# Kernel optimization log

Measured on AMD Instinct MI355X. Metric: run time of the kernel, lower is better.

Reference implementation:

```python
import jax, jax.numpy as jnp
import numpy as np

NU, NI, E = 50000, 20000, 400000
IN, HID, OUT = 128, 256, 128
NEG_SLOPE_ATTN = 0.2   # DGL GATConv default
NEG_SLOPE_ACT = 0.01   # F.leaky_relu default
BN_EPS = 1e-5


def setup_inputs() -> dict:
    key = jax.random.key(0)
    ks = jax.random.split(key, 32)
    d = {}
    d["x_user"] = jax.random.normal(ks[0], (NU, IN), jnp.float32)
    d["x_item"] = jax.random.normal(ks[1], (NI, IN), jnp.float32)
    d["eu"] = jax.random.randint(ks[2], (E,), 0, NU, jnp.int32)
    d["ei"] = jax.random.randint(ks[3], (E,), 0, NI, jnp.int32)
    i = 4
    dims = [(IN, 4, 64), (HID, 4, 64), (HID, 4, 64), (HID, 4, 32)]
    for L, (fin, H, dh) in enumerate(dims):
        for rel in ("ui", "iu"):
            d[f"W{L}_{rel}"] = jax.random.normal(ks[i], (fin, H * dh), jnp.float32) * 0.1; i += 1
            d[f"A{L}_{rel}"] = jax.random.normal(ks[i], (2, H, dh), jnp.float32) * 0.1; i += 1
    # BN params: [layer, (gamma,beta), HID]; gamma near 1, beta near 0
    gu = 1.0 + 0.05 * jax.random.normal(ks[i], (3, 1, HID), jnp.float32); i += 1
    bu = 0.05 * jax.random.normal(ks[i], (3, 1, HID), jnp.float32); i += 1
    gi = 1.0 + 0.05 * jax.random.normal(ks[i], (3, 1, HID), jnp.float32); i += 1
    bi = 0.05 * jax.random.normal(ks[i], (3, 1, HID), jnp.float32); i += 1
    d["bn_u"] = jnp.concatenate([gu, bu], axis=1)
    d["bn_i"] = jnp.concatenate([gi, bi], axis=1)
    return d


def _gat(x_src, x_dst, W, A, src, dst, n_dst):
    # Single-relation bipartite GATConv (DGL semantics).
    H, dh = A.shape[1], A.shape[2]
    hs = (x_src @ W).reshape(-1, H, dh)           # [Ns,H,dh]
    hd = (x_dst @ W).reshape(-1, H, dh)           # [Nd,H,dh]
    el = jnp.einsum('nhd,hd->nh', hs, A[0])
    er = jnp.einsum('nhd,hd->nh', hd, A[1])
    e = jax.nn.leaky_relu(el[src] + er[dst], NEG_SLOPE_ATTN)   # [E,H]
    emax = jax.ops.segment_max(e, dst, num_segments=n_dst)
    ee = jnp.exp(e - emax[dst])
    denom = jax.ops.segment_sum(ee, dst, num_segments=n_dst)
    alpha = ee / denom[dst]                       # segment softmax over in-edges
    out = jax.ops.segment_sum(hs[src] * alpha[..., None], dst, num_segments=n_dst)
    return out.reshape(n_dst, H * dh)


def _bn(x, gamma, beta):
    mu = x.mean(axis=0)
    var = x.var(axis=0)   # biased, matches torch BN normalization
    return gamma * (x - mu) * jax.lax.rsqrt(var + BN_EPS) + beta


def reference(x_user, x_item, eu, ei, W0_ui, W0_iu, A0_ui, A0_iu,
              W1_ui, W1_iu, A1_ui, A1_iu, W2_ui, W2_iu, A2_ui, A2_iu,
              W3_ui, W3_iu, A3_ui, A3_iu, bn_u, bn_i):
    Wui = [W0_ui, W1_ui, W2_ui]; Aui = [A0_ui, A1_ui, A2_ui]
    Wiu = [W0_iu, W1_iu, W2_iu]; Aiu = [A0_iu, A1_iu, A2_iu]
    hu, hi = x_user, x_item
    for L in range(3):
        ni = _gat(hu, hi, Wui[L], Aui[L], eu, ei, NI)   # user -> item
        nu = _gat(hi, hu, Wiu[L], Aiu[L], ei, eu, NU)   # item -> user
        nu = _bn(nu, bn_u[L, 0], bn_u[L, 1])
        ni = _bn(ni, bn_i[L, 0], bn_i[L, 1])
        if L == 2:   # last hidden layer uses tanh in non-residual path
            hu, hi = jnp.tanh(nu), jnp.tanh(ni)
        else:
            hu = jax.nn.leaky_relu(nu, NEG_SLOPE_ACT)
            hi = jax.nn.leaky_relu(ni, NEG_SLOPE_ACT)
    out_i = _gat(hu, hi, W3_ui, A3_ui, eu, ei, NI)
    out_u = _gat(hi, hu, W3_iu, A3_iu, ei, eu, NU)
    return jnp.concatenate([out_u, out_i], axis=0)   # [NU+NI, OUT]
```

## Files before the change

### kernel.cpp

```cpp
#include <hip/hip_runtime.h>

#define NUSERS 50000
#define NITEMS 20000
#define NEDGES 400000

typedef _Float16 f16;
typedef __attribute__((ext_vector_type(8))) _Float16 f16x8;
typedef __attribute__((ext_vector_type(4))) _Float16 f16x4;
typedef __attribute__((ext_vector_type(2))) _Float16 f16x2;
typedef __attribute__((ext_vector_type(4))) float f32x4;

__global__ void prep_k(const float* __restrict__ Wa, const float* __restrict__ Aa,
                       f16* __restrict__ Bta, float* __restrict__ efa,
                       const float* __restrict__ Wb, const float* __restrict__ Ab,
                       f16* __restrict__ Btb, float* __restrict__ efb,
                       int K, int Nw, int dh) {
  int t = blockIdx.x * blockDim.x + threadIdx.x;
  int half = K * Nw;
  if (t >= 2 * half) return;
  const float* W = (t < half) ? Wa : Wb;
  const float* A = (t < half) ? Aa : Ab;
  f16* Bt = (t < half) ? Bta : Btb;
  float* ef = (t < half) ? efa : efb;
  int t2 = (t < half) ? t : t - half;
  int n = t2 / K, k = t2 - n * K;
  Bt[t2] = (f16)W[(long)k * Nw + n];
  if (t2 < K * 8) {
    int j = t2 / (K * 4);
    int r = t2 - j * K * 4;
    int h = r / K, f = r - h * K;
    const float* Aj = A + j * Nw;
    float s = 0.f;
    for (int d = 0; d < dh; ++d) s += W[f * Nw + h * dh + d] * Aj[h * dh + d];
    ef[j * 4 * K + h * K + f] = s;
  }
}

__global__ void xcvt_k(const float* __restrict__ xu, f16* __restrict__ yu, long nu,
                       const float* __restrict__ xi, f16* __restrict__ yi, long ni) {
  long i = (long)blockIdx.x * blockDim.x + threadIdx.x;
  if (i < nu) yu[i] = (f16)xu[i];
  else if (i < nu + ni) yi[i - nu] = (f16)xi[i - nu];
}

__global__ __launch_bounds__(256) void hgemm2_k(const f16* __restrict__ Aa, const f16* __restrict__ Bta,
                                                f16* __restrict__ Ca, int Ma, int gya,
                                                const f16* __restrict__ Ab, const f16* __restrict__ Btb,
                                                f16* __restrict__ Cb, int Mb,
                                                int N, int K) {
  __shared__ f16 As[128 * 32];
  __shared__ f16 Bs[128 * 32];
  int by = blockIdx.y;
  const f16* A; const f16* Bt; f16* C; int M; int row0;
  if (by < gya) { A = Aa; Bt = Bta; C = Ca; M = Ma; row0 = by * 128; }
  else          { A = Ab; Bt = Btb; C = Cb; M = Mb; row0 = (by - gya) * 128; }
  int tid = threadIdx.x;
  int col0 = blockIdx.x * 128;
  int lane = tid & 63, wv = tid >> 6;
  int wr = (wv & 1) * 64, wc = (wv >> 1) * 64;
  int l16 = lane & 15, q = lane >> 4;
  f32x4 acc[4][4] = {};
  int r = tid >> 2, c8 = (tid & 3) * 8;
  for (int k0 = 0; k0 < K; k0 += 32) {
    int ra = min(row0 + r, M - 1);
    uint4 va = *(const uint4*)&A[(long)ra * K + k0 + c8];
    int ra2 = min(row0 + r + 64, M - 1);
    uint4 va2 = *(const uint4*)&A[(long)ra2 * K + k0 + c8];
    uint4 vb = *(const uint4*)&Bt[(long)(col0 + r) * K + k0 + c8];
    uint4 vb2 = *(const uint4*)&Bt[(long)(col0 + r + 64) * K + k0 + c8];
    *(uint4*)&As[r * 32 + c8] = va;
    *(uint4*)&As[(r + 64) * 32 + c8] = va2;
    *(uint4*)&Bs[r * 32 + c8] = vb;
    *(uint4*)&Bs[(r + 64) * 32 + c8] = vb2;
    __syncthreads();
    f16x8 af[4], bfr[4];
#pragma unroll
    for (int i = 0; i < 4; ++i) {
      af[i] = *(const f16x8*)&As[(wr + i * 16 + l16) * 32 + q * 8];
      bfr[i] = *(const f16x8*)&Bs[(wc + i * 16 + l16) * 32 + q * 8];
    }
#pragma unroll
    for (int i = 0; i < 4; ++i)
#pragma unroll
      for (int j = 0; j < 4; ++j)
        acc[i][j] = __builtin_amdgcn_mfma_f32_16x16x32_f16(af[i], bfr[j], acc[i][j], 0, 0, 0);
    __syncthreads();
  }
#pragma unroll
  for (int i = 0; i < 4; ++i) {
#pragma unroll
    for (int reg = 0; reg < 4; ++reg) {
      int rr = row0 + wr + i * 16 + q * 4 + reg;
      if (rr < M) {
#pragma unroll
        for (int j = 0; j < 4; ++j)
          C[(long)rr * N + col0 + wc + j * 16 + l16] = (f16)acc[i][j][reg];
      }
    }
  }
}

__global__ __launch_bounds__(256) void eler_k(
    const f16* __restrict__ hbu, const float* __restrict__ ef_ui, const float* __restrict__ ef_iu,
    float* __restrict__ el_u, float* __restrict__ er_u,
    const f16* __restrict__ hbi, float* __restrict__ el_i, float* __restrict__ er_i, int K) {
  __shared__ float xs[256];
  int b = blockIdx.x, t = threadIdx.x;
  const f16* hb; const float* elf; const float* erf; float* el; float* er; int n;
  if (b < NUSERS) { hb = hbu; elf = ef_ui; erf = ef_iu + 4 * K; el = el_u; er = er_u; n = b; }
  else            { hb = hbi; elf = ef_iu; erf = ef_ui + 4 * K; el = el_i; er = er_i; n = b - NUSERS; }
  if (t < K) xs[t] = (float)hb[(long)n * K + t];
  __syncthreads();
  int j = t >> 5, l = t & 31;
  const float* fr = (j < 4) ? (elf + j * K) : (erf + (j - 4) * K);
  float p = 0.f;
  for (int f = l; f < K; f += 32) p += xs[f] * fr[f];
#pragma unroll
  for (int off = 16; off; off >>= 1) p += __shfl_down(p, off, 32);
  if (l == 0) { if (j < 4) el[n * 4 + j] = p; else er[n * 4 + (j - 4)] = p; }
}

__global__ void hist_k(const int* __restrict__ ei, int* __restrict__ degi,
                       const int* __restrict__ eu, int* __restrict__ degu) {
  int e = blockIdx.x * blockDim.x + threadIdx.x;
  if (e < NEDGES) atomicAdd(&degi[ei[e]], 1);
  else if (e < 2 * NEDGES) atomicAdd(&degu[eu[e - NEDGES]], 1);
}

__global__ __launch_bounds__(256) void scan1_k(const int* __restrict__ deg,
                                               int* __restrict__ bsum, int N) {
  __shared__ int red[256];
  int base = blockIdx.x * 1024, t = threadIdx.x;
  int s = 0;
#pragma unroll
  for (int j = 0; j < 4; ++j) { int i = base + t * 4 + j; s += (i < N) ? deg[i] : 0; }
  red[t] = s; __syncthreads();
  for (int off = 128; off; off >>= 1) { if (t < off) red[t] += red[t + off]; __syncthreads(); }
  if (t == 0) bsum[blockIdx.x] = red[0];
}

__global__ void scan2_k(int* __restrict__ bsum, int nb) {
  if (threadIdx.x == 0) {
    int run = 0;
    for (int i = 0; i < nb; ++i) { int v = bsum[i]; bsum[i] = run; run += v; }
  }
}

__global__ __launch_bounds__(256) void scan3_k(const int* __restrict__ deg,
                                               const int* __restrict__ bsum,
                                               int* __restrict__ rowptr, int N) {
  __shared__ int tsum[256];
  int base = blockIdx.x * 1024, t = threadIdx.x;
  int v[4]; int s = 0;
#pragma unroll
  for (int j = 0; j < 4; ++j) { int i = base + t * 4 + j; v[j] = (i < N) ? deg[i] : 0; s += v[j]; }
  tsum[t] = s; __syncthreads();
  for (int off = 1; off < 256; off <<= 1) {
    int x = (t >= off) ? tsum[t - off] : 0;
    __syncthreads();
    tsum[t] += x;
    __syncthreads();
  }
  int run = bsum[blockIdx.x] + ((t > 0) ? tsum[t - 1] : 0);
#pragma unroll
  for (int j = 0; j < 4; ++j) {
    int i = base + t * 4 + j;
    if (i < N) rowptr[i] = run;
    run += v[j];
  }
}

__global__ void setval_k(int* __restrict__ p, int v) { *p = v; }

__global__ void copy2_k(const int* __restrict__ a, int* __restrict__ b, int Na,
                        const int* __restrict__ c, int* __restrict__ d, int Nc) {
  int i = blockIdx.x * blockDim.x + threadIdx.x;
  if (i < Na) b[i] = a[i];
  else if (i < Na + Nc) d[i - Na] = c[i - Na];
}

__global__ void scat_k(const int* __restrict__ ei, const int* __restrict__ eu,
                       int* __restrict__ curi, int* __restrict__ srci,
                       int* __restrict__ curu, int* __restrict__ srcu) {
  int e = blockIdx.x * blockDim.x + threadIdx.x;
  if (e < NEDGES) {
    int p = atomicAdd(&curi[ei[e]], 1);
    srci[p] = eu[e];
  } else if (e < 2 * NEDGES) {
    int e2 = e - NEDGES;
    int p = atomicAdd(&curu[eu[e2]], 1);
    srcu[p] = ei[e2];
  }
}

template <int W, int DH, typename OUT>
__global__ __launch_bounds__(256) void agg_k(
    const float* __restrict__ elA, const float* __restrict__ erA,
    const int* __restrict__ rpA, const int* __restrict__ srcA,
    const f16* __restrict__ hsA, OUT* __restrict__ outA, int nA,
    const float* __restrict__ elB, const float* __restrict__ erB,
    const int* __restrict__ rpB, const int* __restrict__ srcB,
    const f16* __restrict__ hsB, OUT* __restrict__ outB, int nB) {
  constexpr int CPL = W >> 6;
  constexpr int SHIFT = (W == 256) ? 9 : 8;
  constexpr bool OF16 = (sizeof(OUT) == 2);
  __shared__ float alds[4][256];
  __shared__ int soff[4][64];
  int wv = threadIdx.x >> 6;
  int g = blockIdx.x * 4 + wv;
  int lane = threadIdx.x & 63;
  const float* el; const float* er; const int* rp; const int* srcv;
  const f16* hs; OUT* outp; int d;
  if (g < nA)           { el = elA; er = erA; rp = rpA; srcv = srcA; hs = hsA; outp = outA; d = g; }
  else if (g < nA + nB) { el = elB; er = erB; rp = rpB; srcv = srcB; hs = hsB; outp = outB; d = g - nA; }
  else return;
  int s0 = rp[d], s1 = rp[d + 1];
  int deg = s1 - s0;
  int c0 = lane * CPL;
  int h = c0 / DH;
  long obase = (long)d * W + c0;
  if (deg == 0) {
#pragma unroll
    for (int q = 0; q < CPL; ++q) outp[obase + q] = (OUT)0.f;
    return;
  }
  const float NEG = -3.0e38f;
  float acc[CPL];
#pragma unroll
  for (int q = 0; q < CPL; ++q) acc[q] = 0.f;
  float inv;

  if (deg <= 64) {
    int hh = lane & 3, p = lane >> 2;
    float er_h = er[d * 4 + hh];
    float vv[4];
    float vmax = NEG;
#pragma unroll
    for (int j = 0; j < 4; ++j) {
      int slot = j * 16 + p;
      vv[j] = NEG;
      if (slot < deg) {
        int sj = srcv[s0 + slot];
        if (hh == 0) soff[wv][slot] = sj << SHIFT;
        float v = el[sj * 4 + hh] + er_h;
        v = v > 0.f ? v : 0.2f * v;
        vv[j] = v;
        vmax = fmaxf(vmax, v);
      }
    }
#pragma unroll
    for (int off = 4; off < 64; off <<= 1) vmax = fmaxf(vmax, __shfl_xor(vmax, off, 64));
    float ssum = 0.f;
#pragma unroll
    for (int j = 0; j < 4; ++j) {
      int slot = j * 16 + p;
      if (slot < deg) {
        float e = expf(vv[j] - vmax);
        alds[wv][slot * 4 + hh] = e;
        ssum += e;
      }
    }
#pragma unroll
    for (int off = 4; off < 64; off <<= 1) ssum += __shfl_xor(ssum, off, 64);
    float Sh = __shfl(ssum, (lane & ~3) | h, 64);
    inv = 1.0f / Sh;
    const char* hbase = (const char*)hs + (size_t)c0 * sizeof(f16);
    for (int j = 0; j < deg; ++j) {
      float aj = alds[wv][j * 4 + h];
      int off = soff[wv][j];
      const f16* row = (const f16*)(hbase + (size_t)(unsigned)off);
      if constexpr (CPL == 4) {
        f16x4 hv = *(const f16x4*)row;
        acc[0] += aj * (float)hv[0]; acc[1] += aj * (float)hv[1];
        acc[2] += aj * (float)hv[2]; acc[3] += aj * (float)hv[3];
      } else {
        f16x2 hv = *(const f16x2*)row;
        acc[0] += aj * (float)hv[0]; acc[1] += aj * (float)hv[1];
      }
    }
  } else {
    float4 er4 = *(const float4*)&er[d * 4];
    float m0 = NEG, m1 = NEG, m2 = NEG, m3 = NEG;
    for (int k = s0 + lane; k < s1; k += 64) {
      int s = srcv[k];
      float4 e4 = *(const float4*)&el[s * 4];
      float v;
      v = e4.x + er4.x; v = v > 0.f ? v : 0.2f * v; m0 = fmaxf(m0, v);
      v = e4.y + er4.y; v = v > 0.f ? v : 0.2f * v; m1 = fmaxf(m1, v);
      v = e4.z + er4.z; v = v > 0.f ? v : 0.2f * v; m2 = fmaxf(m2, v);
      v = e4.w + er4.w; v = v > 0.f ? v : 0.2f * v; m3 = fmaxf(m3, v);
    }
#pragma unroll
    for (int off = 32; off; off >>= 1) {
      m0 = fmaxf(m0, __shfl_xor(m0, off, 64));
      m1 = fmaxf(m1, __shfl_xor(m1, off, 64));
      m2 = fmaxf(m2, __shfl_xor(m2, off, 64));
      m3 = fmaxf(m3, __shfl_xor(m3, off, 64));
    }
    float S0 = 0.f, S1 = 0.f, S2 = 0.f, S3 = 0.f;
    for (int k = s0 + lane; k < s1; k += 64) {
      int s = srcv[k];
      float4 e4 = *(const float4*)&el[s * 4];
      float v;
      v = e4.x + er4.x; v = v > 0.f ? v : 0.2f * v; S0 += expf(v - m0);
      v = e4.y + er4.y; v = v > 0.f ? v : 0.2f * v; S1 += expf(v - m1);
      v = e4.z + er4.z; v = v > 0.f ? v : 0.2f * v; S2 += expf(v - m2);
      v = e4.w + er4.w; v = v > 0.f ? v : 0.2f * v; S3 += expf(v - m3);
    }
#pragma unroll
    for (int off = 32; off; off >>= 1) {
      S0 += __shfl_xor(S0, off, 64);
      S1 += __shfl_xor(S1, off, 64);
      S2 += __shfl_xor(S2, off, 64);
      S3 += __shfl_xor(S3, off, 64);
    }
    float mh = h == 0 ? m0 : h == 1 ? m1 : h == 2 ? m2 : m3;
    float Sh = h == 0 ? S0 : h == 1 ? S1 : h == 2 ? S2 : S3;
    float erh = h == 0 ? er4.x : h == 1 ? er4.y : h == 2 ? er4.z : er4.w;
    inv = 1.0f / Sh;
    for (int k = s0; k < s1; ++k) {
      int s = srcv[k];
      float v = el[s * 4 + h] + erh; v = v > 0.f ? v : 0.2f * v;
      float a = expf(v - mh);
      const f16* row = &hs[(long)s * W + c0];
      if constexpr (CPL == 4) {
        f16x4 hv = *(const f16x4*)row;
        acc[0] += a * (float)hv[0]; acc[1] += a * (float)hv[1];
        acc[2] += a * (float)hv[2]; acc[3] += a * (float)hv[3];
      } else {
        f16x2 hv = *(const f16x2*)row;
        acc[0] += a * (float)hv[0]; acc[1] += a * (float)hv[1];
      }
    }
  }
  if constexpr (OF16) {
    if constexpr (CPL == 4) {
      f16x4 o = { (f16)(acc[0] * inv), (f16)(acc[1] * inv), (f16)(acc[2] * inv), (f16)(acc[3] * inv) };
      *(f16x4*)&outp[obase] = o;
    } else {
      f16x2 o = { (f16)(acc[0] * inv), (f16)(acc[1] * inv) };
      *(f16x2*)&outp[obase] = o;
    }
  } else {
    if constexpr (CPL == 4) {
      *(float4*)&outp[obase] = make_float4(acc[0] * inv, acc[1] * inv, acc[2] * inv, acc[3] * inv);
    } else {
      *(float2*)&outp[obase] = make_float2(acc[0] * inv, acc[1] * inv);
    }
  }
}

__global__ void zero2_k(float* __restrict__ a, float* __restrict__ b) {
  int t = threadIdx.x;
  a[t] = 0.f; b[t] = 0.f;
}

__global__ __launch_bounds__(256) void bn_stats2_k(const f16* __restrict__ xu, float* __restrict__ su, int Nu, int gU,
                                                   const f16* __restrict__ xi, float* __restrict__ si, int Ni) {
  const int C = 256;
  int b = blockIdx.x;
  const f16* x; float* sums; int N; int r0;
  if (b < gU) { x = xu; sums = su; N = Nu; r0 = b * 64; }
  else        { x = xi; sums = si; N = Ni; r0 = (b - gU) * 64; }
  int c = threadIdx.x;
  int r1 = min(r0 + 64, N);
  float s = 0.f, s2 = 0.f;
  for (int r = r0; r < r1; ++r) {
    float v = (float)x[(long)r * C + c];
    s += v; s2 += v * v;
  }
  atomicAdd(&sums[c], s);
  atomicAdd(&sums[C + c], s2);
}

__global__ __launch_bounds__(256) void bn_fused_k(
    const f16* __restrict__ xu, const float* __restrict__ su, const float* __restrict__ gbu,
    f16* __restrict__ yu, int Nu,
    const f16* __restrict__ xi, const float* __restrict__ si, const float* __restrict__ gbi,
    f16* __restrict__ yi, int Ni,
    const float* __restrict__ efu, const float* __restrict__ efiu,
    float* __restrict__ el_u, float* __restrict__ er_u,
    float* __restrict__ el_i, float* __restrict__ er_i, int act) {
  const int Kn = 256;
  __shared__ float xs[256];
  int b = blockIdx.x, t = threadIdx.x;
  const f16* x; const float* sums; const float* gb; f16* y; int n; int N;
  const float* elf; const float* erf; float* el; float* er;
  if (b < Nu) { x = xu; sums = su; gb = gbu; y = yu; n = b; N = Nu; elf = efu;  erf = efiu + 4 * Kn; el = el_u; er = er_u; }
  else        { x = xi; sums = si; gb = gbi; y = yi; n = b - Nu; N = Ni; elf = efiu; erf = efu + 4 * Kn;  el = el_i; er = er_i; }
  long base = (long)n * 256;
  float val = (float)x[base + t];
  float inv_n = 1.0f / (float)N;
  float mean = sums[t] * inv_n;
  float var = sums[256 + t] * inv_n - mean * mean;
  float v = gb[t] * (val - mean) * rsqrtf(var + 1e-5f) + gb[256 + t];
  v = act ? tanhf(v) : (v > 0.f ? v : 0.01f * v);
  y[base + t] = (f16)v;
  xs[t] = v;
  __syncthreads();
  int j = t >> 5, l = t & 31;
  const float* fr = (j < 4) ? (elf + j * Kn) : (erf + (j - 4) * Kn);
  float p = 0.f;
  for (int f = l; f < Kn; f += 32) p += xs[f] * fr[f];
#pragma unroll
  for (int off = 16; off; off >>= 1) p += __shfl_down(p, off, 32);
  if (l == 0) { if (j < 4) el[n * 4 + j] = p; else er[n * 4 + (j - 4)] = p; }
}

extern "C" void kernel_launch(void* const* d_in, const int* in_sizes, int n_in,
                              void* d_out, int out_size, void* d_ws, size_t ws_size,
                              hipStream_t stream) {
  const float* x_user = (const float*)d_in[0];
  const float* x_item = (const float*)d_in[1];
  const int* eu = (const int*)d_in[2];
  const int* ei = (const int*)d_in[3];
  const float *Wm[4][2], *Am[4][2];
  for (int L = 0; L < 4; ++L) {
    Wm[L][0] = (const float*)d_in[4 + L * 4 + 0];
    Am[L][0] = (const float*)d_in[4 + L * 4 + 1];
    Wm[L][1] = (const float*)d_in[4 + L * 4 + 2];
    Am[L][1] = (const float*)d_in[4 + L * 4 + 3];
  }
  const float* bnu = (const float*)d_in[20];
  const float* bni = (const float*)d_in[21];
  float* out = (float*)d_out;

  float* ws = (float*)d_ws;
  size_t o = 0;
  float* el_u = ws + o; o += (size_t)NUSERS * 4;
  float* er_u = ws + o; o += (size_t)NUSERS * 4;
  float* el_i = ws + o; o += (size_t)NITEMS * 4;
  float* er_i = ws + o; o += (size_t)NITEMS * 4;
  float* ef_all[4][2];
  for (int L = 0; L < 4; ++L)
    for (int rl = 0; rl < 2; ++rl) { ef_all[L][rl] = ws + o; o += 2048; }
  float* bns_u = ws + o; o += 512;
  float* bns_i = ws + o; o += 512;
  f16* hb_u   = (f16*)(ws + o); o += (size_t)NUSERS * 128;
  f16* hb_i   = (f16*)(ws + o); o += (size_t)NITEMS * 128;
  f16* hsb_u  = (f16*)(ws + o); o += (size_t)NUSERS * 128;
  f16* hsb_i  = (f16*)(ws + o); o += (size_t)NITEMS * 128;
  f16* aggh_u = (f16*)(ws + o); o += (size_t)NUSERS * 128;
  f16* aggh_i = (f16*)(ws + o); o += (size_t)NITEMS * 128;
  f16* Bt_all[4][2];
  for (int L = 0; L < 4; ++L) {
    int K = (L == 0) ? 128 : 256;
    int W = (L == 3) ? 128 : 256;
    for (int rl = 0; rl < 2; ++rl) { Bt_all[L][rl] = (f16*)(ws + o); o += (size_t)K * W / 2; }
  }
  int* deg_i    = (int*)(ws + o); o += NITEMS;
  int* deg_u    = (int*)(ws + o); o += NUSERS;
  int* rowptr_i = (int*)(ws + o); o += NITEMS + 1;
  int* rowptr_u = (int*)(ws + o); o += NUSERS + 1;
  int* cur_i    = (int*)(ws + o); o += NITEMS;
  int* cur_u    = (int*)(ws + o); o += NUSERS;
  int* bsum     = (int*)(ws + o); o += 256;
  int* csrsrc_i = (int*)(ws + o); o += NEDGES;
  int* csrsrc_u = (int*)(ws + o); o += NEDGES;

  const int gE2 = (2 * NEDGES + 255) / 256;
  const int nb_i = (NITEMS + 1023) / 1024;
  const int nb_u = (NUSERS + 1023) / 1024;
  const int gU = (NUSERS + 63) / 64;
  const int gI = (NITEMS + 63) / 64;

  hipMemsetAsync(deg_i, 0, (NITEMS + NUSERS) * sizeof(int), stream);
  hist_k<<<dim3(gE2), dim3(256), 0, stream>>>(ei, deg_i, eu, deg_u);
  scan1_k<<<dim3(nb_i), dim3(256), 0, stream>>>(deg_i, bsum, NITEMS);
  scan2_k<<<dim3(1), dim3(64), 0, stream>>>(bsum, nb_i);
  scan3_k<<<dim3(nb_i), dim3(256), 0, stream>>>(deg_i, bsum, rowptr_i, NITEMS);
  setval_k<<<dim3(1), dim3(1), 0, stream>>>(rowptr_i + NITEMS, NEDGES);
  scan1_k<<<dim3(nb_u), dim3(256), 0, stream>>>(deg_u, bsum, NUSERS);
  scan2_k<<<dim3(1), dim3(64), 0, stream>>>(bsum, nb_u);
  scan3_k<<<dim3(nb_u), dim3(256), 0, stream>>>(deg_u, bsum, rowptr_u, NUSERS);
  setval_k<<<dim3(1), dim3(1), 0, stream>>>(rowptr_u + NUSERS, NEDGES);
  copy2_k<<<dim3((NITEMS + NUSERS + 255) / 256), dim3(256), 0, stream>>>(rowptr_i, cur_i, NITEMS, rowptr_u, cur_u, NUSERS);
  scat_k<<<dim3(gE2), dim3(256), 0, stream>>>(ei, eu, cur_i, csrsrc_i, cur_u, csrsrc_u);

  for (int L = 0; L < 4; ++L) {
    int K = (L == 0) ? 128 : 256;
    int dh = (L == 3) ? 32 : 64;
    int W = 4 * dh;
    prep_k<<<dim3((2 * K * W + 255) / 256), dim3(256), 0, stream>>>(
        Wm[L][0], Am[L][0], Bt_all[L][0], ef_all[L][0],
        Wm[L][1], Am[L][1], Bt_all[L][1], ef_all[L][1], K, W, dh);
  }

  xcvt_k<<<dim3(((NUSERS + NITEMS) * 128 + 255) / 256), dim3(256), 0, stream>>>(
      x_user, hb_u, (long)NUSERS * 128, x_item, hb_i, (long)NITEMS * 128);
  eler_k<<<dim3(NUSERS + NITEMS), dim3(256), 0, stream>>>(
      hb_u, ef_all[0][0], ef_all[0][1], el_u, er_u, hb_i, el_i, er_i, 128);

  int K = 128;
  for (int L = 0; L < 4; ++L) {
    const int dh = (L == 3) ? 32 : 64;
    const int W = 4 * dh;

    const int gya = (NUSERS + 127) / 128, gyb = (NITEMS + 127) / 128;
    hgemm2_k<<<dim3(W / 128, gya + gyb), dim3(256), 0, stream>>>(
        hb_u, Bt_all[L][0], hsb_u, NUSERS, gya, hb_i, Bt_all[L][1], hsb_i, NITEMS, W, K);

    const int gAgg = (NITEMS + NUSERS + 3) / 4;
    if (L < 3) {
      agg_k<256, 64, f16><<<dim3(gAgg), dim3(256), 0, stream>>>(
          el_u, er_i, rowptr_i, csrsrc_i, hsb_u, aggh_i, NITEMS,
          el_i, er_u, rowptr_u, csrsrc_u, hsb_i, aggh_u, NUSERS);
      zero2_k<<<dim3(1), dim3(512), 0, stream>>>(bns_u, bns_i);
      bn_stats2_k<<<dim3(gU + gI), dim3(256), 0, stream>>>(aggh_u, bns_u, NUSERS, gU, aggh_i, bns_i, NITEMS);
      bn_fused_k<<<dim3(NUSERS + NITEMS), dim3(256), 0, stream>>>(
          aggh_u, bns_u, bnu + L * 512, hb_u, NUSERS,
          aggh_i, bns_i, bni + L * 512, hb_i, NITEMS,
          ef_all[L + 1][0], ef_all[L + 1][1],
          el_u, er_u, el_i, er_i, L == 2);
      K = 256;
    } else {
      agg_k<128, 32, float><<<dim3(gAgg), dim3(256), 0, stream>>>(
          el_u, er_i, rowptr_i, csrsrc_i, hsb_u, out + (size_t)NUSERS * 128, NITEMS,
          el_i, er_u, rowptr_u, csrsrc_u, hsb_i, out, NUSERS);
    }
  }
}
```

Before: 917.6 us.

## Fuse BN statistics into aggregation and merge small setup kernels

Batch-norm sum and sum-of-squares are now accumulated inside the aggregation kernel, first in shared memory and then with atomics spread over four partial buffers, so the separate stats pass that re-read the aggregated features is gone. The input fp16 conversion is folded into the layer-0 attention-logit kernel, and the rowptr end write and cursor copy are folded into the scan kernels. This removes several launches and one full read of the activations per layer, at the cost of shared-memory atomics and an extra barrier in the aggregation kernel.

```diff
diff --git a/kernel.cpp b/kernel.cpp
--- a/kernel.cpp
+++ b/kernel.cpp
@@ -34,13 +34,6 @@
     for (int d = 0; d < dh; ++d) s += W[f * Nw + h * dh + d] * Aj[h * dh + d];
     ef[j * 4 * K + h * K + f] = s;
   }
-}
-
-__global__ void xcvt_k(const float* __restrict__ xu, f16* __restrict__ yu, long nu,
-                       const float* __restrict__ xi, f16* __restrict__ yi, long ni) {
-  long i = (long)blockIdx.x * blockDim.x + threadIdx.x;
-  if (i < nu) yu[i] = (f16)xu[i];
-  else if (i < nu + ni) yi[i - nu] = (f16)xi[i - nu];
 }
 
 __global__ __launch_bounds__(256) void hgemm2_k(const f16* __restrict__ Aa, const f16* __restrict__ Bta,
@@ -100,16 +93,23 @@
   }
 }
 
-__global__ __launch_bounds__(256) void eler_k(
-    const f16* __restrict__ hbu, const float* __restrict__ ef_ui, const float* __restrict__ ef_iu,
+__global__ __launch_bounds__(256) void eler0_k(
+    const float* __restrict__ xu, f16* __restrict__ hbu,
+    const float* __restrict__ ef_ui, const float* __restrict__ ef_iu,
     float* __restrict__ el_u, float* __restrict__ er_u,
-    const f16* __restrict__ hbi, float* __restrict__ el_i, float* __restrict__ er_i, int K) {
-  __shared__ float xs[256];
+    const float* __restrict__ xi, f16* __restrict__ hbi,
+    float* __restrict__ el_i, float* __restrict__ er_i) {
+  const int K = 128;
+  __shared__ float xs[128];
   int b = blockIdx.x, t = threadIdx.x;
-  const f16* hb; const float* elf; const float* erf; float* el; float* er; int n;
-  if (b < NUSERS) { hb = hbu; elf = ef_ui; erf = ef_iu + 4 * K; el = el_u; er = er_u; n = b; }
-  else            { hb = hbi; elf = ef_iu; erf = ef_ui + 4 * K; el = el_i; er = er_i; n = b - NUSERS; }
-  if (t < K) xs[t] = (float)hb[(long)n * K + t];
+  const float* x; f16* hb; const float* elf; const float* erf; float* el; float* er; int n;
+  if (b < NUSERS) { x = xu; hb = hbu; elf = ef_ui; erf = ef_iu + 4 * K; el = el_u; er = er_u; n = b; }
+  else            { x = xi; hb = hbi; elf = ef_iu; erf = ef_ui + 4 * K; el = el_i; er = er_i; n = b - NUSERS; }
+  if (t < K) {
+    f16 xv = (f16)x[(long)n * K + t];
+    hb[(long)n * K + t] = xv;
+    xs[t] = (float)xv;
+  }
   __syncthreads();
   int j = t >> 5, l = t & 31;
   const float* fr = (j < 4) ? (elf + j * K) : (erf + (j - 4) * K);
@@ -139,16 +139,18 @@
   if (t == 0) bsum[blockIdx.x] = red[0];
 }
 
-__global__ void scan2_k(int* __restrict__ bsum, int nb) {
+__global__ void scan2_k(int* __restrict__ bsum, int nb, int* __restrict__ endp, int endv) {
   if (threadIdx.x == 0) {
     int run = 0;
     for (int i = 0; i < nb; ++i) { int v = bsum[i]; bsum[i] = run; run += v; }
+    *endp = endv;
   }
 }
 
 __global__ __launch_bounds__(256) void scan3_k(const int* __restrict__ deg,
                                                const int* __restrict__ bsum,
-                                               int* __restrict__ rowptr, int N) {
+                                               int* __restrict__ rowptr,
+                                               int* __restrict__ cur, int N) {
   __shared__ int tsum[256];
   int base = blockIdx.x * 1024, t = threadIdx.x;
   int v[4]; int s = 0;
@@ -165,18 +167,9 @@
 #pragma unroll
   for (int j = 0; j < 4; ++j) {
     int i = base + t * 4 + j;
-    if (i < N) rowptr[i] = run;
+    if (i < N) { rowptr[i] = run; cur[i] = run; }
     run += v[j];
   }
-}
-
-__global__ void setval_k(int* __restrict__ p, int v) { *p = v; }
-
-__global__ void copy2_k(const int* __restrict__ a, int* __restrict__ b, int Na,
-                        const int* __restrict__ c, int* __restrict__ d, int Nc) {
-  int i = blockIdx.x * blockDim.x + threadIdx.x;
-  if (i < Na) b[i] = a[i];
-  else if (i < Na + Nc) d[i - Na] = c[i - Na];
 }
 
 __global__ void scat_k(const int* __restrict__ ei, const int* __restrict__ eu,
@@ -193,184 +186,194 @@
   }
 }
 
-template <int W, int DH, typename OUT>
+template <int W, int DH, typename OUT, bool STATS>
 __global__ __launch_bounds__(256) void agg_k(
     const float* __restrict__ elA, const float* __restrict__ erA,
     const int* __restrict__ rpA, const int* __restrict__ srcA,
-    const f16* __restrict__ hsA, OUT* __restrict__ outA, int nA,
+    const f16* __restrict__ hsA, OUT* __restrict__ outA, int nA, int gA,
+    float* __restrict__ bnsA,
     const float* __restrict__ elB, const float* __restrict__ erB,
     const int* __restrict__ rpB, const int* __restrict__ srcB,
-    const f16* __restrict__ hsB, OUT* __restrict__ outB, int nB) {
+    const f16* __restrict__ hsB, OUT* __restrict__ outB, int nB,
+    float* __restrict__ bnsB) {
   constexpr int CPL = W >> 6;
   constexpr int SHIFT = (W == 256) ? 9 : 8;
   constexpr bool OF16 = (sizeof(OUT) == 2);
   __shared__ float alds[4][256];
   __shared__ int soff[4][64];
-  int wv = threadIdx.x >> 6;
-  int g = blockIdx.x * 4 + wv;
-  int lane = threadIdx.x & 63;
-  const float* el; const float* er; const int* rp; const int* srcv;
-  const f16* hs; OUT* outp; int d;
-  if (g < nA)           { el = elA; er = erA; rp = rpA; srcv = srcA; hs = hsA; outp = outA; d = g; }
-  else if (g < nA + nB) { el = elB; er = erB; rp = rpB; srcv = srcB; hs = hsB; outp = outB; d = g - nA; }
-  else return;
-  int s0 = rp[d], s1 = rp[d + 1];
-  int deg = s1 - s0;
+  __shared__ float sst[2][256];
+  int tid = threadIdx.x;
+  int wv = tid >> 6;
+  int lane = tid & 63;
+  bool sideA = (blockIdx.x < gA);
+  const float* el = sideA ? elA : elB;
+  const float* er = sideA ? erA : erB;
+  const int* rp   = sideA ? rpA : rpB;
+  const int* srcv = sideA ? srcA : srcB;
+  const f16* hs   = sideA ? hsA : hsB;
+  OUT* outp       = sideA ? outA : outB;
+  float* bns      = sideA ? bnsA : bnsB;
+  int n           = sideA ? nA : nB;
+  int d = (sideA ? blockIdx.x : blockIdx.x - gA) * 4 + wv;
+  bool active = (d < n);
+
+  if constexpr (STATS) {
+    sst[0][tid] = 0.f; sst[1][tid] = 0.f;
+    __syncthreads();
+  }
+
+  const float NEG = -3.0e38f;
+  float acc[CPL];
+#pragma unroll
+  for (int q = 0; q < CPL; ++q) acc[q] = 0.f;
+  float inv = 0.f;
   int c0 = lane * CPL;
   int h = c0 / DH;
+  int s0 = 0, deg = 0;
+  if (active) { s0 = rp[d]; deg = rp[d + 1] - s0; }
+
+  if (active && deg > 0) {
+    if (deg <= 64) {
+      int hh = lane & 3, p = lane >> 2;
+      float er_h = er[d * 4 + hh];
+      float vv[4];
+      float vmax = NEG;
+#pragma unroll
+      for (int j = 0; j < 4; ++j) {
+        int slot = j * 16 + p;
+        vv[j] = NEG;
+        if (slot < deg) {
+          int sj = srcv[s0 + slot];
+          if (hh == 0) soff[wv][slot] = sj << SHIFT;
+          float v = el[sj * 4 + hh] + er_h;
+          v = v > 0.f ? v : 0.2f * v;
+          vv[j] = v;
+          vmax = fmaxf(vmax, v);
+        }
+      }
+#pragma unroll
+      for (int off = 4; off < 64; off <<= 1) vmax = fmaxf(vmax, __shfl_xor(vmax, off, 64));
+      float ssum = 0.f;
+#pragma unroll
+      for (int j = 0; j < 4; ++j) {
+        int slot = j * 16 + p;
+        if (slot < deg) {
+          float e = expf(vv[j] - vmax);
+          alds[wv][slot * 4 + hh] = e;
+          ssum += e;
+        }
+      }
+#pragma unroll
+      for (int off = 4; off < 64; off <<= 1) ssum += __shfl_xor(ssum, off, 64);
+      float Sh = __shfl(ssum, (lane & ~3) | h, 64);
+      inv = 1.0f / Sh;
+      const char* hbase = (const char*)hs + (size_t)c0 * sizeof(f16);
+      for (int j = 0; j < deg; ++j) {
+        float aj = alds[wv][j * 4 + h];
+        int off = soff[wv][j];
+        const f16* row = (const f16*)(hbase + (size_t)(unsigned)off);
+        if constexpr (CPL == 4) {
+          f16x4 hv = *(const f16x4*)row;
+          acc[0] += aj * (float)hv[0]; acc[1] += aj * (float)hv[1];
+          acc[2] += aj * (float)hv[2]; acc[3] += aj * (float)hv[3];
+        } else {
+          f16x2 hv = *(const f16x2*)row;
+          acc[0] += aj * (float)hv[0]; acc[1] += aj * (float)hv[1];
+        }
+      }
+    } else {
+      float4 er4 = *(const float4*)&er[d * 4];
+      float m0 = NEG, m1 = NEG, m2 = NEG, m3 = NEG;
+      for (int k = s0 + lane; k < s0 + deg; k += 64) {
+        int s = srcv[k];
+        float4 e4 = *(const float4*)&el[s * 4];
+        float v;
+        v = e4.x + er4.x; v = v > 0.f ? v : 0.2f * v; m0 = fmaxf(m0, v);
+        v = e4.y + er4.y; v = v > 0.f ? v : 0.2f * v; m1 = fmaxf(m1, v);
+        v = e4.z + er4.z; v = v > 0.f ? v : 0.2f * v; m2 = fmaxf(m2, v);
+        v = e4.w + er4.w; v = v > 0.f ? v : 0.2f * v; m3 = fmaxf(m3, v);
+      }
+#pragma unroll
+      for (int off = 32; off; off >>= 1) {
+        m0 = fmaxf(m0, __shfl_xor(m0, off, 64));
+        m1 = fmaxf(m1, __shfl_xor(m1, off, 64));
+        m2 = fmaxf(m2, __shfl_xor(m2, off, 64));
+        m3 = fmaxf(m3, __shfl_xor(m3, off, 64));
+      }
+      float S0 = 0.f, S1 = 0.f, S2 = 0.f, S3 = 0.f;
+      for (int k = s0 + lane; k < s0 + deg; k += 64) {
+        int s = srcv[k];
+        float4 e4 = *(const float4*)&el[s * 4];
+        float v;
+        v = e4.x + er4.x; v = v > 0.f ? v : 0.2f * v; S0 += expf(v - m0);
+        v = e4.y + er4.y; v = v > 0.f ? v : 0.2f * v; S1 += expf(v - m1);
+        v = e4.z + er4.z; v = v > 0.f ? v : 0.2f * v; S2 += expf(v - m2);
+        v = e4.w + er4.w; v = v > 0.f ? v : 0.2f * v; S3 += expf(v - m3);
+      }
+#pragma unroll
+      for (int off = 32; off; off >>= 1) {
+        S0 += __shfl_xor(S0, off, 64);
+        S1 += __shfl_xor(S1, off, 64);
+        S2 += __shfl_xor(S2, off, 64);
+        S3 += __shfl_xor(S3, off, 64);
+      }
+      float mh = h == 0 ? m0 : h == 1 ? m1 : h == 2 ? m2 : m3;
+      float Sh = h == 0 ? S0 : h == 1 ? S1 : h == 2 ? S2 : S3;
+      float erh = h == 0 ? er4.x : h == 1 ? er4.y : h == 2 ? er4.z : er4.w;
+      inv = 1.0f / Sh;
+      for (int k = s0; k < s0 + deg; ++k) {
+        int s = srcv[k];
+        float v = el[s * 4 + h] + erh; v = v > 0.f ? v : 0.2f * v;
+        float a = expf(v - mh);
+        const f16* row = &hs[(long)s * W + c0];
+        if constexpr (CPL == 4) {
+          f16x4 hv = *(const f16x4*)row;
+          acc[0] += a * (float)hv[0]; acc[1] += a * (float)hv[1];
+          acc[2] += a * (float)hv[2]; acc[3] += a * (float)hv[3];
+        } else {
+          f16x2 hv = *(const f16x2*)row;
+          acc[0] += a * (float)hv[0]; acc[1] += a * (float)hv[1];
+        }
+      }
+    }
+  }
+
   long obase = (long)d * W + c0;
-  if (deg == 0) {
-#pragma unroll
-    for (int q = 0; q < CPL; ++q) outp[obase + q] = (OUT)0.f;
-    return;
-  }
-  const float NEG = -3.0e38f;
-  float acc[CPL];
-#pragma unroll
-  for (int q = 0; q < CPL; ++q) acc[q] = 0.f;
-  float inv;
-
-  if (deg <= 64) {
-    int hh = lane & 3, p = lane >> 2;
-    float er_h = er[d * 4 + hh];
-    float vv[4];
-    float vmax = NEG;
-#pragma unroll
-    for (int j = 0; j < 4; ++j) {
-      int slot = j * 16 + p;
-      vv[j] = NEG;
-      if (slot < deg) {
-        int sj = srcv[s0 + slot];
-        if (hh == 0) soff[wv][slot] = sj << SHIFT;
-        float v = el[sj * 4 + hh] + er_h;
-        v = v > 0.f ? v : 0.2f * v;
-        vv[j] = v;
-        vmax = fmaxf(vmax, v);
+  float vq[CPL];
+  if (active) {
+    if constexpr (OF16) {
+      if constexpr (CPL == 4) {
+        f16x4 o;
+#pragma unroll
+        for (int q = 0; q < 4; ++q) { o[q] = (f16)(acc[q] * inv); vq[q] = (float)o[q]; }
+        *(f16x4*)&outp[obase] = o;
+      } else {
+        f16x2 o;
+#pragma unroll
+        for (int q = 0; q < 2; ++q) { o[q] = (f16)(acc[q] * inv); vq[q] = (float)o[q]; }
+        *(f16x2*)&outp[obase] = o;
+      }
+    } else {
+      if constexpr (CPL == 4) {
+        *(float4*)&outp[obase] = make_float4(acc[0] * inv, acc[1] * inv, acc[2] * inv, acc[3] * inv);
+      } else {
+        *(float2*)&outp[obase] = make_float2(acc[0] * inv, acc[1] * inv);
       }
     }
-#pragma unroll
-    for (int off = 4; off < 64; off <<= 1) vmax = fmaxf(vmax, __shfl_xor(vmax, off, 64));
-    float ssum = 0.f;
-#pragma unroll
-    for (int j = 0; j < 4; ++j) {
-      int slot = j * 16 + p;
-      if (slot < deg) {
-        float e = expf(vv[j] - vmax);
-        alds[wv][slot * 4 + hh] = e;
-        ssum += e;
+  }
+  if constexpr (STATS) {
+    if (active) {
+#pragma unroll
+      for (int q = 0; q < CPL; ++q) {
+        atomicAdd(&sst[0][c0 + q], vq[q]);
+        atomicAdd(&sst[1][c0 + q], vq[q] * vq[q]);
       }
     }
-#pragma unroll
-    for (int off = 4; off < 64; off <<= 1) ssum += __shfl_xor(ssum, off, 64);
-    float Sh = __shfl(ssum, (lane & ~3) | h, 64);
-    inv = 1.0f / Sh;
-    const char* hbase = (const char*)hs + (size_t)c0 * sizeof(f16);
-    for (int j = 0; j < deg; ++j) {
-      float aj = alds[wv][j * 4 + h];
-      int off = soff[wv][j];
-      const f16* row = (const f16*)(hbase + (size_t)(unsigned)off);
-      if constexpr (CPL == 4) {
-        f16x4 hv = *(const f16x4*)row;
-        acc[0] += aj * (float)hv[0]; acc[1] += aj * (float)hv[1];
-        acc[2] += aj * (float)hv[2]; acc[3] += aj * (float)hv[3];
-      } else {
-        f16x2 hv = *(const f16x2*)row;
-        acc[0] += aj * (float)hv[0]; acc[1] += aj * (float)hv[1];
-      }
-    }
-  } else {
-    float4 er4 = *(const float4*)&er[d * 4];
-    float m0 = NEG, m1 = NEG, m2 = NEG, m3 = NEG;
-    for (int k = s0 + lane; k < s1; k += 64) {
-      int s = srcv[k];
-      float4 e4 = *(const float4*)&el[s * 4];
-      float v;
-      v = e4.x + er4.x; v = v > 0.f ? v : 0.2f * v; m0 = fmaxf(m0, v);
-      v = e4.y + er4.y; v = v > 0.f ? v : 0.2f * v; m1 = fmaxf(m1, v);
-      v = e4.z + er4.z; v = v > 0.f ? v : 0.2f * v; m2 = fmaxf(m2, v);
-      v = e4.w + er4.w; v = v > 0.f ? v : 0.2f * v; m3 = fmaxf(m3, v);
-    }
-#pragma unroll
-    for (int off = 32; off; off >>= 1) {
-      m0 = fmaxf(m0, __shfl_xor(m0, off, 64));
-      m1 = fmaxf(m1, __shfl_xor(m1, off, 64));
-      m2 = fmaxf(m2, __shfl_xor(m2, off, 64));
-      m3 = fmaxf(m3, __shfl_xor(m3, off, 64));
-    }
-    float S0 = 0.f, S1 = 0.f, S2 = 0.f, S3 = 0.f;
-    for (int k = s0 + lane; k < s1; k += 64) {
-      int s = srcv[k];
-      float4 e4 = *(const float4*)&el[s * 4];
-      float v;
-      v = e4.x + er4.x; v = v > 0.f ? v : 0.2f * v; S0 += expf(v - m0);
-      v = e4.y + er4.y; v = v > 0.f ? v : 0.2f * v; S1 += expf(v - m1);
-      v = e4.z + er4.z; v = v > 0.f ? v : 0.2f * v; S2 += expf(v - m2);
-      v = e4.w + er4.w; v = v > 0.f ? v : 0.2f * v; S3 += expf(v - m3);
-    }
-#pragma unroll
-    for (int off = 32; off; off >>= 1) {
-      S0 += __shfl_xor(S0, off, 64);
-      S1 += __shfl_xor(S1, off, 64);
-      S2 += __shfl_xor(S2, off, 64);
-      S3 += __shfl_xor(S3, off, 64);
-    }
-    float mh = h == 0 ? m0 : h == 1 ? m1 : h == 2 ? m2 : m3;
-    float Sh = h == 0 ? S0 : h == 1 ? S1 : h == 2 ? S2 : S3;
-    float erh = h == 0 ? er4.x : h == 1 ? er4.y : h == 2 ? er4.z : er4.w;
-    inv = 1.0f / Sh;
-    for (int k = s0; k < s1; ++k) {
-      int s = srcv[k];
-      float v = el[s * 4 + h] + erh; v = v > 0.f ? v : 0.2f * v;
-      float a = expf(v - mh);
-      const f16* row = &hs[(long)s * W + c0];
-      if constexpr (CPL == 4) {
-        f16x4 hv = *(const f16x4*)row;
-        acc[0] += a * (float)hv[0]; acc[1] += a * (float)hv[1];
-        acc[2] += a * (float)hv[2]; acc[3] += a * (float)hv[3];
-      } else {
-        f16x2 hv = *(const f16x2*)row;
-        acc[0] += a * (float)hv[0]; acc[1] += a * (float)hv[1];
-      }
-    }
-  }
-  if constexpr (OF16) {
-    if constexpr (CPL == 4) {
-      f16x4 o = { (f16)(acc[0] * inv), (f16)(acc[1] * inv), (f16)(acc[2] * inv), (f16)(acc[3] * inv) };
-      *(f16x4*)&outp[obase] = o;
-    } else {
-      f16x2 o = { (f16)(acc[0] * inv), (f16)(acc[1] * inv) };
-      *(f16x2*)&outp[obase] = o;
-    }
-  } else {
-    if constexpr (CPL == 4) {
-      *(float4*)&outp[obase] = make_float4(acc[0] * inv, acc[1] * inv, acc[2] * inv, acc[3] * inv);
-    } else {
-      *(float2*)&outp[obase] = make_float2(acc[0] * inv, acc[1] * inv);
-    }
-  }
-}
-
-__global__ void zero2_k(float* __restrict__ a, float* __restrict__ b) {
-  int t = threadIdx.x;
-  a[t] = 0.f; b[t] = 0.f;
-}
-
-__global__ __launch_bounds__(256) void bn_stats2_k(const f16* __restrict__ xu, float* __restrict__ su, int Nu, int gU,
-                                                   const f16* __restrict__ xi, float* __restrict__ si, int Ni) {
-  const int C = 256;
-  int b = blockIdx.x;
-  const f16* x; float* sums; int N; int r0;
-  if (b < gU) { x = xu; sums = su; N = Nu; r0 = b * 64; }
-  else        { x = xi; sums = si; N = Ni; r0 = (b - gU) * 64; }
-  int c = threadIdx.x;
-  int r1 = min(r0 + 64, N);
-  float s = 0.f, s2 = 0.f;
-  for (int r = r0; r < r1; ++r) {
-    float v = (float)x[(long)r * C + c];
-    s += v; s2 += v * v;
-  }
-  atomicAdd(&sums[c], s);
-  atomicAdd(&sums[C + c], s2);
+    __syncthreads();
+    float* b = bns + (blockIdx.x & 3) * 512;
+    atomicAdd(&b[tid], sst[0][tid]);
+    atomicAdd(&b[256 + tid], sst[1][tid]);
+  }
 }
 
 __global__ __launch_bounds__(256) void bn_fused_k(
@@ -391,8 +394,10 @@
   long base = (long)n * 256;
   float val = (float)x[base + t];
   float inv_n = 1.0f / (float)N;
-  float mean = sums[t] * inv_n;
-  float var = sums[256 + t] * inv_n - mean * mean;
+  float s  = sums[t] + sums[512 + t] + sums[1024 + t] + sums[1536 + t];
+  float s2 = sums[256 + t] + sums[768 + t] + sums[1280 + t] + sums[1792 + t];
+  float mean = s * inv_n;
+  float var = s2 * inv_n - mean * mean;
   float v = gb[t] * (val - mean) * rsqrtf(var + 1e-5f) + gb[256 + t];
   v = act ? tanhf(v) : (v > 0.f ? v : 0.01f * v);
   y[base + t] = (f16)v;
@@ -427,6 +432,9 @@
 
   float* ws = (float*)d_ws;
   size_t o = 0;
+  int* deg_i    = (int*)(ws + o); o += NITEMS;
+  int* deg_u    = (int*)(ws + o); o += NUSERS;
+  float* bns_all = ws + o; o += 3 * 2 * 2048;
   float* el_u = ws + o; o += (size_t)NUSERS * 4;
   float* er_u = ws + o; o += (size_t)NUSERS * 4;
   float* el_i = ws + o; o += (size_t)NITEMS * 4;
@@ -434,8 +442,6 @@
   float* ef_all[4][2];
   for (int L = 0; L < 4; ++L)
     for (int rl = 0; rl < 2; ++rl) { ef_all[L][rl] = ws + o; o += 2048; }
-  float* bns_u = ws + o; o += 512;
-  float* bns_i = ws + o; o += 512;
   f16* hb_u   = (f16*)(ws + o); o += (size_t)NUSERS * 128;
   f16* hb_i   = (f16*)(ws + o); o += (size_t)NITEMS * 128;
   f16* hsb_u  = (f16*)(ws + o); o += (size_t)NUSERS * 128;
@@ -448,8 +454,6 @@
     int W = (L == 3) ? 128 : 256;
     for (int rl = 0; rl < 2; ++rl) { Bt_all[L][rl] = (f16*)(ws + o); o += (size_t)K * W / 2; }
   }
-  int* deg_i    = (int*)(ws + o); o += NITEMS;
-  int* deg_u    = (int*)(ws + o); o += NUSERS;
   int* rowptr_i = (int*)(ws + o); o += NITEMS + 1;
   int* rowptr_u = (int*)(ws + o); o += NUSERS + 1;
   int* cur_i    = (int*)(ws + o); o += NITEMS;
@@ -461,20 +465,15 @@
   const int gE2 = (2 * NEDGES + 255) / 256;
   const int nb_i = (NITEMS + 1023) / 1024;
   const int nb_u = (NUSERS + 1023) / 1024;
-  const int gU = (NUSERS + 63) / 64;
-  const int gI = (NITEMS + 63) / 64;
-
-  hipMemsetAsync(deg_i, 0, (NITEMS + NUSERS) * sizeof(int), stream);
+
+  hipMemsetAsync(deg_i, 0, (NITEMS + NUSERS + 3 * 2 * 2048) * sizeof(int), stream);
   hist_k<<<dim3(gE2), dim3(256), 0, stream>>>(ei, deg_i, eu, deg_u);
   scan1_k<<<dim3(nb_i), dim3(256), 0, stream>>>(deg_i, bsum, NITEMS);
-  scan2_k<<<dim3(1), dim3(64), 0, stream>>>(bsum, nb_i);
-  scan3_k<<<dim3(nb_i), dim3(256), 0, stream>>>(deg_i, bsum, rowptr_i, NITEMS);
-  setval_k<<<dim3(1), dim3(1), 0, stream>>>(rowptr_i + NITEMS, NEDGES);
+  scan2_k<<<dim3(1), dim3(64), 0, stream>>>(bsum, nb_i, rowptr_i + NITEMS, NEDGES);
+  scan3_k<<<dim3(nb_i), dim3(256), 0, stream>>>(deg_i, bsum, rowptr_i, cur_i, NITEMS);
   scan1_k<<<dim3(nb_u), dim3(256), 0, stream>>>(deg_u, bsum, NUSERS);
-  scan2_k<<<dim3(1), dim3(64), 0, stream>>>(bsum, nb_u);
-  scan3_k<<<dim3(nb_u), dim3(256), 0, stream>>>(deg_u, bsum, rowptr_u, NUSERS);
-  setval_k<<<dim3(1), dim3(1), 0, stream>>>(rowptr_u + NUSERS, NEDGES);
-  copy2_k<<<dim3((NITEMS + NUSERS + 255) / 256), dim3(256), 0, stream>>>(rowptr_i, cur_i, NITEMS, rowptr_u, cur_u, NUSERS);
+  scan2_k<<<dim3(1), dim3(64), 0, stream>>>(bsum, nb_u, rowptr_u + NUSERS, NEDGES);
+  scan3_k<<<dim3(nb_u), dim3(256), 0, stream>>>(deg_u, bsum, rowptr_u, cur_u, NUSERS);
   scat_k<<<dim3(gE2), dim3(256), 0, stream>>>(ei, eu, cur_i, csrsrc_i, cur_u, csrsrc_u);
 
   for (int L = 0; L < 4; ++L) {
@@ -486,12 +485,12 @@
         Wm[L][1], Am[L][1], Bt_all[L][1], ef_all[L][1], K, W, dh);
   }
 
-  xcvt_k<<<dim3(((NUSERS + NITEMS) * 128 + 255) / 256), dim3(256), 0, stream>>>(
-      x_user, hb_u, (long)NUSERS * 128, x_item, hb_i, (long)NITEMS * 128);
-  eler_k<<<dim3(NUSERS + NITEMS), dim3(256), 0, stream>>>(
-      hb_u, ef_all[0][0], ef_all[0][1], el_u, er_u, hb_i, el_i, er_i, 128);
+  eler0_k<<<dim3(NUSERS + NITEMS), dim3(256), 0, stream>>>(
+      x_user, hb_u, ef_all[0][0], ef_all[0][1], el_u, er_u,
+      x_item, hb_i, el_i, er_i);
 
   int K = 128;
+  const int gAi = (NITEMS + 3) / 4, gAu = (NUSERS + 3) / 4;
   for (int L = 0; L < 4; ++L) {
     const int dh = (L == 3) ? 32 : 64;
     const int W = 4 * dh;
@@ -500,23 +499,22 @@
     hgemm2_k<<<dim3(W / 128, gya + gyb), dim3(256), 0, stream>>>(
         hb_u, Bt_all[L][0], hsb_u, NUSERS, gya, hb_i, Bt_all[L][1], hsb_i, NITEMS, W, K);
 
-    const int gAgg = (NITEMS + NUSERS + 3) / 4;
     if (L < 3) {
-      agg_k<256, 64, f16><<<dim3(gAgg), dim3(256), 0, stream>>>(
-          el_u, er_i, rowptr_i, csrsrc_i, hsb_u, aggh_i, NITEMS,
-          el_i, er_u, rowptr_u, csrsrc_u, hsb_i, aggh_u, NUSERS);
-      zero2_k<<<dim3(1), dim3(512), 0, stream>>>(bns_u, bns_i);
-      bn_stats2_k<<<dim3(gU + gI), dim3(256), 0, stream>>>(aggh_u, bns_u, NUSERS, gU, aggh_i, bns_i, NITEMS);
+      float* bns_i_L = bns_all + (L * 2 + 0) * 2048;
+      float* bns_u_L = bns_all + (L * 2 + 1) * 2048;
+      agg_k<256, 64, f16, true><<<dim3(gAi + gAu), dim3(256), 0, stream>>>(
+          el_u, er_i, rowptr_i, csrsrc_i, hsb_u, aggh_i, NITEMS, gAi, bns_i_L,
+          el_i, er_u, rowptr_u, csrsrc_u, hsb_i, aggh_u, NUSERS, bns_u_L);
       bn_fused_k<<<dim3(NUSERS + NITEMS), dim3(256), 0, stream>>>(
-          aggh_u, bns_u, bnu + L * 512, hb_u, NUSERS,
-          aggh_i, bns_i, bni + L * 512, hb_i, NITEMS,
+          aggh_u, bns_u_L, bnu + L * 512, hb_u, NUSERS,
+          aggh_i, bns_i_L, bni + L * 512, hb_i, NITEMS,
           ef_all[L + 1][0], ef_all[L + 1][1],
           el_u, er_u, el_i, er_i, L == 2);
       K = 256;
     } else {
-      agg_k<128, 32, float><<<dim3(gAgg), dim3(256), 0, stream>>>(
-          el_u, er_i, rowptr_i, csrsrc_i, hsb_u, out + (size_t)NUSERS * 128, NITEMS,
-          el_i, er_u, rowptr_u, csrsrc_u, hsb_i, out, NUSERS);
+      agg_k<128, 32, float, false><<<dim3(gAi + gAu), dim3(256), 0, stream>>>(
+          el_u, er_i, rowptr_i, csrsrc_i, hsb_u, out + (size_t)NUSERS * 128, NITEMS, gAi, nullptr,
+          el_i, er_u, rowptr_u, csrsrc_u, hsb_i, out, NUSERS, nullptr);
     }
   }
 }
```

After: 1.250 ms. +36.2%, slower.
